# Kernel tuning notes

Hardware: AMD Instinct MI355X
Metric: run time of the kernel (lower is better)

Reference implementation:

```python
import jax, jax.numpy as jnp
import numpy as np

N_SRC0, N_DST0 = 500000, 65536
N_DST1 = 8192
E0, E1 = 1048576, 131072
H = 4
SLOPE = 0.2


def gat_conv(h_src, h_dst, src, dst, Ws, Wd, al, ar, b, n_dst, act):
    # h_src: [Ns, Fin], Ws: [Fin, H*D]
    D = Ws.shape[1] // H
    fs = (h_src @ Ws).reshape(-1, H, D)          # [Ns,H,D]
    fd = (h_dst @ Wd).reshape(-1, H, D)          # [Nd,H,D]
    el = jnp.einsum('nhd,hd->nh', fs, al)        # [Ns,H]
    er = jnp.einsum('nhd,hd->nh', fd, ar)        # [Nd,H]
    e = jax.nn.leaky_relu(el[src] + er[dst], SLOPE)   # [E,H]
    m = jax.ops.segment_max(e, dst, num_segments=n_dst, indices_are_sorted=True)
    a = jnp.exp(e - m[dst])                      # [E,H]
    s = jax.ops.segment_sum(a, dst, num_segments=n_dst, indices_are_sorted=True)
    alpha = a / s[dst]                           # [E,H]
    msg = fs[src] * alpha[..., None]             # [E,H,D]
    out = jax.ops.segment_sum(msg, dst, num_segments=n_dst, indices_are_sorted=True) + b
    return act(out)                              # [Nd,H,D]


def setup_inputs() -> dict:
    key = jax.random.key(0)
    ks = jax.random.split(key, 16)
    D0, D1 = 64, 47
    inp = {
        'x': jax.random.normal(ks[0], (N_SRC0, 128), jnp.float32),
        'src0': jax.random.randint(ks[1], (E0,), 0, N_SRC0, jnp.int32),
        'dst0': jnp.sort(jax.random.randint(ks[2], (E0,), 0, N_DST0, jnp.int32)),
        'src1': jax.random.randint(ks[3], (E1,), 0, N_DST0, jnp.int32),
        'dst1': jnp.sort(jax.random.randint(ks[4], (E1,), 0, N_DST1, jnp.int32)),
        'Ws0': jax.random.normal(ks[5], (128, H * D0), jnp.float32) * 0.05,
        'Wd0': jax.random.normal(ks[6], (128, H * D0), jnp.float32) * 0.05,
        'al0': jax.random.normal(ks[7], (H, D0), jnp.float32) * 0.05,
        'ar0': jax.random.normal(ks[8], (H, D0), jnp.float32) * 0.05,
        'b0': jax.random.normal(ks[9], (H, D0), jnp.float32) * 0.05,
        'Ws1': jax.random.normal(ks[10], (H * D0, H * D1), jnp.float32) * 0.05,
        'Wd1': jax.random.normal(ks[11], (H * D0, H * D1), jnp.float32) * 0.05,
        'al1': jax.random.normal(ks[12], (H, D1), jnp.float32) * 0.05,
        'ar1': jax.random.normal(ks[13], (H, D1), jnp.float32) * 0.05,
        'b1': jax.random.normal(ks[14], (H, D1), jnp.float32) * 0.05,
    }
    return inp


def reference(x, src0, dst0, src1, dst1, Ws0, Wd0, al0, ar0, b0, Ws1, Wd1, al1, ar1, b1):
    # Layer 0: bipartite GATConv with ReLU, flatten heads
    h_dst = x[:N_DST0]
    h = gat_conv(x, h_dst, src0, dst0, Ws0, Wd0, al0, ar0, b0, N_DST0, jax.nn.relu)
    h = h.reshape(N_DST0, -1)                    # [N_DST0, H*D0]
    # Layer 1: no activation, mean over heads, log_softmax
    h_dst = h[:N_DST1]
    h = gat_conv(h, h_dst, src1, dst1, Ws1, Wd1, al1, ar1, b1, N_DST1, lambda z: z)
    h = h.mean(axis=1)                           # [N_DST1, D1]
    return jax.nn.log_softmax(h, axis=-1)
```

## Files before the change

kernel.cpp:

```cpp
#include <hip/hip_runtime.h>

typedef _Float16 half8  __attribute__((ext_vector_type(8)));
typedef _Float16 half4v __attribute__((ext_vector_type(4)));
typedef float    f32x4  __attribute__((ext_vector_type(4)));

#define GAT_SLOPE 0.2f
#define N_SRC0 500000
#define N_DST0 65536
#define N_DST1 8192
#define E0 1048576
#define E1 131072
#define H 4

__device__ __forceinline__ float leaky(float x) { return x >= 0.f ? x : GAT_SLOPE * x; }

__global__ __launch_bounds__(256) void prep_kernel(
    const float* __restrict__ Ws0, const float* __restrict__ Wd0,
    const float* __restrict__ al0, const float* __restrict__ ar0,
    const float* __restrict__ Ws1, const float* __restrict__ Wd1,
    const float* __restrict__ al1, const float* __restrict__ ar1,
    const int* __restrict__ dst0, const int* __restrict__ dst1,
    _Float16* __restrict__ BTs, _Float16* __restrict__ BT0,
    _Float16* __restrict__ WLR0, float* __restrict__ wl1, float* __restrict__ wr1,
    int* __restrict__ seg0, int* __restrict__ seg1) {
  int i = blockIdx.x * 256 + threadIdx.x;
  if (i < 65536) {
    int n = i >> 10, kk = i & 1023, h = kk >> 8, k = kk & 255;
    BTs[i] = (n < 47) ? (_Float16)(0.25f * Ws1[(size_t)k * 188 + h * 47 + n]) : (_Float16)0.f;
    return;
  }
  i -= 65536;
  if (i < 32768) {
    int nrow = i >> 7, k = i & 127;
    BT0[i] = (_Float16)Ws0[(size_t)k * 256 + nrow];
    return;
  }
  i -= 32768;
  if (i < 2048) {
    int n = i >> 7, k = i & 127;
    float v = 0.f;
    if (n < 4) {
      for (int d = 0; d < 64; ++d) v += Ws0[(size_t)k * 256 + n * 64 + d] * al0[n * 64 + d];
    } else if (n < 8) {
      int h = n - 4;
      for (int d = 0; d < 64; ++d) v += Wd0[(size_t)k * 256 + h * 64 + d] * ar0[h * 64 + d];
    }
    WLR0[i] = (_Float16)v;
    return;
  }
  i -= 2048;
  if (i < 1024) {
    int k = i >> 2, h = i & 3;
    float v = 0.f;
    for (int d = 0; d < 47; ++d) v += Ws1[(size_t)k * 188 + h * 47 + d] * al1[h * 47 + d];
    wl1[i] = v;
    return;
  }
  i -= 1024;
  if (i < 1024) {
    int k = i >> 2, h = i & 3;
    float v = 0.f;
    for (int d = 0; d < 47; ++d) v += Wd1[(size_t)k * 188 + h * 47 + d] * ar1[h * 47 + d];
    wr1[i] = v;
    return;
  }
  i -= 1024;
  if (i <= E0) {
    int lo = (i == 0) ? 0 : dst0[i - 1] + 1;
    int hi = (i == E0) ? N_DST0 : dst0[i];
    for (int d = lo; d <= hi; ++d) seg0[d] = i;
    return;
  }
  i -= (E0 + 1);
  if (i <= E1) {
    int lo = (i == 0) ? 0 : dst1[i - 1] + 1;
    int hi = (i == E1) ? N_DST1 : dst1[i];
    for (int d = lo; d <= hi; ++d) seg1[d] = i;
  }
}
#define PREP_TOTAL (65536 + 32768 + 2048 + 1024 + 1024 + (E0 + 1) + (E1 + 1))

__global__ __launch_bounds__(256) void cvt_elr_mfma_kernel(
    const float* __restrict__ x, const _Float16* __restrict__ WLR,
    _Float16* __restrict__ xh, float* __restrict__ el, float* __restrict__ er,
    int M, int n_dst) {
  __shared__ _Float16 As[128 * 128];
  const int t = threadIdx.x, lane = t & 63, wid = t >> 6;
  const int m0 = blockIdx.x * 128;
  for (int i = 0; i < 8; ++i) {
    int c = t + 256 * i;
    int row = c >> 4, j = c & 15;
    int gr = m0 + row;
    half8 va = {};
    if (gr < M) {
      float4 f0 = *(const float4*)(x + (size_t)gr * 128 + j * 8);
      float4 f1 = *(const float4*)(x + (size_t)gr * 128 + j * 8 + 4);
      va[0] = (_Float16)f0.x; va[1] = (_Float16)f0.y;
      va[2] = (_Float16)f0.z; va[3] = (_Float16)f0.w;
      va[4] = (_Float16)f1.x; va[5] = (_Float16)f1.y;
      va[6] = (_Float16)f1.z; va[7] = (_Float16)f1.w;
      *(half8*)(xh + (size_t)gr * 128 + j * 8) = va;
    }
    *(half8*)(&As[row * 128 + ((j ^ (row & 7)) << 3)]) = va;
  }
  half8 bf[4];
  for (int kc = 0; kc < 4; ++kc)
    bf[kc] = *(const half8*)(WLR + (lane & 15) * 128 + kc * 32 + (lane >> 4) * 8);
  __syncthreads();
  f32x4 acc[2] = {};
  for (int rt = 0; rt < 2; ++rt) {
    int row = (wid * 2 + rt) * 16 + (lane & 15);
    for (int kc = 0; kc < 4; ++kc) {
      int chunk = kc * 4 + (lane >> 4);
      half8 af = *(const half8*)(&As[row * 128 + ((chunk ^ (row & 7)) << 3)]);
      acc[rt] = __builtin_amdgcn_mfma_f32_16x16x32_f16(af, bf[kc], acc[rt], 0, 0, 0);
    }
  }
  int col = lane & 15, quad = lane >> 4;
  for (int rt = 0; rt < 2; ++rt)
    for (int r = 0; r < 4; ++r) {
      int row = m0 + (wid * 2 + rt) * 16 + quad * 4 + r;
      if (row < M) {
        if (col < 4) el[(size_t)row * 4 + col] = acc[rt][r];
        else if (col < 8 && row < n_dst) er[(size_t)row * 4 + col - 4] = acc[rt][r];
      }
    }
}

__global__ __launch_bounds__(256) void agg0s_kernel(
    const int* __restrict__ src, const int* __restrict__ seg,
    const float* __restrict__ el, const float* __restrict__ er,
    const _Float16* __restrict__ xh, _Float16* __restrict__ axh) {
  const int lane = threadIdx.x & 63, w = threadIdx.x >> 6;
  const int n = blockIdx.x * 4 + w;
  int s0 = seg[n], len = seg[n + 1] - s0;
  float4 erv = *(const float4*)(er + (size_t)n * 4);
  float a0 = 0.f, a1 = 0.f, a2 = 0.f, a3 = 0.f;
  float t0 = 0.f, t1 = 0.f, t2 = 0.f, t3 = 0.f;
  int sreg = 0;
  if (lane < len) {
    sreg = src[s0 + lane];
    float4 e4 = *(const float4*)(el + (size_t)sreg * 4);
    a0 = __expf(leaky(e4.x + erv.x)); a1 = __expf(leaky(e4.y + erv.y));
    a2 = __expf(leaky(e4.z + erv.z)); a3 = __expf(leaky(e4.w + erv.w));
    t0 = a0; t1 = a1; t2 = a2; t3 = a3;
  }
  for (int idx = 64 + lane; idx < len; idx += 64) {
    int s = src[s0 + idx];
    float4 e4 = *(const float4*)(el + (size_t)s * 4);
    t0 += __expf(leaky(e4.x + erv.x)); t1 += __expf(leaky(e4.y + erv.y));
    t2 += __expf(leaky(e4.z + erv.z)); t3 += __expf(leaky(e4.w + erv.w));
  }
#pragma unroll
  for (int off = 32; off; off >>= 1) {
    t0 += __shfl_xor(t0, off); t1 += __shfl_xor(t1, off);
    t2 += __shfl_xor(t2, off); t3 += __shfl_xor(t3, off);
  }
  float si0 = t0 > 0.f ? 1.f / t0 : 0.f;
  float si1 = t1 > 0.f ? 1.f / t1 : 0.f;
  float si2 = t2 > 0.f ? 1.f / t2 : 0.f;
  float si3 = t3 > 0.f ? 1.f / t3 : 0.f;
  const int g = lane >> 5, ci = lane & 31;
  float A[4][4] = {};
  int iters = (len + 1) >> 1;
  for (int k = 0; k < iters; ++k) {
    int idx = g + 2 * k;
    int sl = idx < 64 ? idx : 0;
    float ah0 = __shfl(a0, sl), ah1 = __shfl(a1, sl);
    float ah2 = __shfl(a2, sl), ah3 = __shfl(a3, sl);
    int sidx = __shfl(sreg, sl);
    if (idx >= 64 && idx < len) {
      sidx = src[s0 + idx];
      float4 e4 = *(const float4*)(el + (size_t)sidx * 4);
      ah0 = __expf(leaky(e4.x + erv.x)); ah1 = __expf(leaky(e4.y + erv.y));
      ah2 = __expf(leaky(e4.z + erv.z)); ah3 = __expf(leaky(e4.w + erv.w));
    }
    if (idx < len) {
      half4v xv = *(const half4v*)(xh + (size_t)sidx * 128 + ci * 4);
#pragma unroll
      for (int c = 0; c < 4; ++c) {
        float xc = (float)xv[c];
        A[0][c] += ah0 * xc; A[1][c] += ah1 * xc;
        A[2][c] += ah2 * xc; A[3][c] += ah3 * xc;
      }
    }
  }
#pragma unroll
  for (int h = 0; h < 4; ++h)
#pragma unroll
    for (int c = 0; c < 4; ++c) A[h][c] += __shfl_xor(A[h][c], 32);
  if (g == 0) {
    float si[4] = {si0, si1, si2, si3};
#pragma unroll
    for (int h = 0; h < 4; ++h) {
      half4v o;
#pragma unroll
      for (int c = 0; c < 4; ++c) o[c] = (_Float16)(A[h][c] * si[h]);
      *(half4v*)(axh + ((size_t)n * 4 + h) * 128 + ci * 4) = o;
    }
  }
}

__global__ __launch_bounds__(256) void agg1s_kernel(
    const int* __restrict__ src, const int* __restrict__ seg,
    const float* __restrict__ el, const float* __restrict__ er,
    const _Float16* __restrict__ h0, _Float16* __restrict__ axh1) {
  const int lane = threadIdx.x & 63, w = threadIdx.x >> 6;
  const int n = blockIdx.x * 4 + w;
  int s0 = seg[n], len = seg[n + 1] - s0;
  float4 erv = *(const float4*)(er + (size_t)n * 4);
  float a0 = 0.f, a1 = 0.f, a2 = 0.f, a3 = 0.f;
  float t0 = 0.f, t1 = 0.f, t2 = 0.f, t3 = 0.f;
  int sreg = 0;
  if (lane < len) {
    sreg = src[s0 + lane];
    float4 e4 = *(const float4*)(el + (size_t)sreg * 4);
    a0 = __expf(leaky(e4.x + erv.x)); a1 = __expf(leaky(e4.y + erv.y));
    a2 = __expf(leaky(e4.z + erv.z)); a3 = __expf(leaky(e4.w + erv.w));
    t0 = a0; t1 = a1; t2 = a2; t3 = a3;
  }
  for (int idx = 64 + lane; idx < len; idx += 64) {
    int s = src[s0 + idx];
    float4 e4 = *(const float4*)(el + (size_t)s * 4);
    t0 += __expf(leaky(e4.x + erv.x)); t1 += __expf(leaky(e4.y + erv.y));
    t2 += __expf(leaky(e4.z + erv.z)); t3 += __expf(leaky(e4.w + erv.w));
  }
#pragma unroll
  for (int off = 32; off; off >>= 1) {
    t0 += __shfl_xor(t0, off); t1 += __shfl_xor(t1, off);
    t2 += __shfl_xor(t2, off); t3 += __shfl_xor(t3, off);
  }
  float si0 = t0 > 0.f ? 1.f / t0 : 0.f;
  float si1 = t1 > 0.f ? 1.f / t1 : 0.f;
  float si2 = t2 > 0.f ? 1.f / t2 : 0.f;
  float si3 = t3 > 0.f ? 1.f / t3 : 0.f;
  const int g = lane >> 5, ci = lane & 31;
  float A[4][8] = {};
  int iters = (len + 1) >> 1;
  for (int k = 0; k < iters; ++k) {
    int idx = g + 2 * k;
    int sl = idx < 64 ? idx : 0;
    float ah0 = __shfl(a0, sl), ah1 = __shfl(a1, sl);
    float ah2 = __shfl(a2, sl), ah3 = __shfl(a3, sl);
    int sidx = __shfl(sreg, sl);
    if (idx >= 64 && idx < len) {
      sidx = src[s0 + idx];
      float4 e4 = *(const float4*)(el + (size_t)sidx * 4);
      ah0 = __expf(leaky(e4.x + erv.x)); ah1 = __expf(leaky(e4.y + erv.y));
      ah2 = __expf(leaky(e4.z + erv.z)); ah3 = __expf(leaky(e4.w + erv.w));
    }
    if (idx < len) {
      half8 xv = *(const half8*)(h0 + (size_t)sidx * 256 + ci * 8);
#pragma unroll
      for (int c = 0; c < 8; ++c) {
        float xc = (float)xv[c];
        A[0][c] += ah0 * xc; A[1][c] += ah1 * xc;
        A[2][c] += ah2 * xc; A[3][c] += ah3 * xc;
      }
    }
  }
#pragma unroll
  for (int h = 0; h < 4; ++h)
#pragma unroll
    for (int c = 0; c < 8; ++c) A[h][c] += __shfl_xor(A[h][c], 32);
  if (g == 0) {
    float si[4] = {si0, si1, si2, si3};
#pragma unroll
    for (int h = 0; h < 4; ++h) {
      half8 o;
#pragma unroll
      for (int c = 0; c < 8; ++c) o[c] = (_Float16)(A[h][c] * si[h]);
      *(half8*)(axh1 + ((size_t)n * 4 + h) * 256 + ci * 8) = o;
    }
  }
}

__global__ __launch_bounds__(256) void gemm_h0_kernel(
    const _Float16* __restrict__ axh, const _Float16* __restrict__ BT,
    const float* __restrict__ b, const float* __restrict__ wl1,
    const float* __restrict__ wr1, _Float16* __restrict__ h0,
    float* __restrict__ el1, float* __restrict__ er1) {
  __shared__ _Float16 As[128 * 128];
  __shared__ _Float16 Bs[64 * 128];
  const int t = threadIdx.x, lane = t & 63, wid = t >> 6;
  const int m0 = blockIdx.x * 128;
  const int cl = lane & 15, quad = lane >> 4;
  const int wm = wid * 32;
  f32x4 el1p[2][4] = {}, er1p[2][4] = {};
  for (int h = 0; h < 4; ++h) {
    for (int i = 0; i < 8; ++i) {
      int c = t + 256 * i, row = c >> 4, j = c & 15;
      int sw = ((j ^ (row & 7)) << 3);
      *(half8*)(&As[row * 128 + sw]) =
          *(const half8*)(axh + ((size_t)(m0 + row) * 4 + h) * 128 + j * 8);
    }
    for (int i = 0; i < 4; ++i) {
      int c = t + 256 * i, row = c >> 4, j = c & 15;
      int sw = ((j ^ (row & 7)) << 3);
      *(half8*)(&Bs[row * 128 + sw]) =
          *(const half8*)(BT + (size_t)(h * 64 + row) * 128 + j * 8);
    }
    __syncthreads();
    f32x4 acc[2][4] = {};
    for (int ks = 0; ks < 4; ++ks) {
      int kc = ks * 4 + quad;
      half8 af[2], bf[4];
      for (int i = 0; i < 2; ++i) {
        int ra = wm + 16 * i + cl;
        af[i] = *(const half8*)(&As[ra * 128 + ((kc ^ (ra & 7)) << 3)]);
      }
      for (int j2 = 0; j2 < 4; ++j2) {
        int rb = 16 * j2 + cl;
        bf[j2] = *(const half8*)(&Bs[rb * 128 + ((kc ^ (rb & 7)) << 3)]);
      }
      for (int i = 0; i < 2; ++i)
        for (int j2 = 0; j2 < 4; ++j2)
          acc[i][j2] = __builtin_amdgcn_mfma_f32_16x16x32_f16(af[i], bf[j2], acc[i][j2], 0, 0, 0);
    }
    __syncthreads();
    for (int j2 = 0; j2 < 4; ++j2) {
      int gcol = h * 64 + 16 * j2 + cl;
      float bias = b[gcol];
      f32x4 wlv = *(const f32x4*)(wl1 + (size_t)gcol * 4);
      f32x4 wrv = *(const f32x4*)(wr1 + (size_t)gcol * 4);
      for (int i = 0; i < 2; ++i) {
        int r0 = m0 + wm + 16 * i + quad * 4;
        for (int r = 0; r < 4; ++r) {
          float v = fmaxf(acc[i][j2][r] + bias, 0.f);
          h0[(size_t)(r0 + r) * 256 + gcol] = (_Float16)v;
          el1p[i][r] += wlv * v;
          er1p[i][r] += wrv * v;
        }
      }
    }
  }
#pragma unroll
  for (int off = 1; off < 16; off <<= 1)
#pragma unroll
    for (int i = 0; i < 2; ++i)
#pragma unroll
      for (int r = 0; r < 4; ++r)
#pragma unroll
        for (int c = 0; c < 4; ++c) {
          el1p[i][r][c] += __shfl_xor(el1p[i][r][c], off);
          er1p[i][r][c] += __shfl_xor(er1p[i][r][c], off);
        }
  if (cl == 0) {
    for (int i = 0; i < 2; ++i)
      for (int r = 0; r < 4; ++r) {
        int row = m0 + wm + 16 * i + quad * 4 + r;
        *(f32x4*)(el1 + (size_t)row * 4) = el1p[i][r];
        if (row < N_DST1) *(f32x4*)(er1 + (size_t)row * 4) = er1p[i][r];
      }
  }
}

__global__ __launch_bounds__(256) void gemm_out_kernel(
    const _Float16* __restrict__ axh1, const _Float16* __restrict__ BTs,
    const float* __restrict__ b1, float* __restrict__ out) {
  __shared__ _Float16 As[64 * 128];
  __shared__ _Float16 Bs[64 * 128];
  const int t = threadIdx.x, lane = t & 63, wid = t >> 6;
  const int m0 = blockIdx.x * 64;
  f32x4 acc[4] = {};
  for (int k0 = 0; k0 < 1024; k0 += 128) {
    for (int i = 0; i < 4; ++i) {
      int c = t + 256 * i, row = c >> 4, j = c & 15;
      int sw = ((j ^ (row & 7)) << 3);
      *(half8*)(&As[row * 128 + sw]) =
          *(const half8*)(axh1 + (size_t)(m0 + row) * 1024 + k0 + j * 8);
      *(half8*)(&Bs[row * 128 + sw]) =
          *(const half8*)(BTs + (size_t)row * 1024 + k0 + j * 8);
    }
    __syncthreads();
    const int wm = wid * 16;
    for (int ks = 0; ks < 4; ++ks) {
      int kc = ks * 4 + (lane >> 4);
      int ra = wm + (lane & 15);
      half8 af = *(const half8*)(&As[ra * 128 + ((kc ^ (ra & 7)) << 3)]);
      for (int j2 = 0; j2 < 4; ++j2) {
        int rb = 16 * j2 + (lane & 15);
        half8 bf = *(const half8*)(&Bs[rb * 128 + ((kc ^ (rb & 7)) << 3)]);
        acc[j2] = __builtin_amdgcn_mfma_f32_16x16x32_f16(af, bf, acc[j2], 0, 0, 0);
      }
    }
    __syncthreads();
  }
  int quad = lane >> 4, cl = lane & 15;
  float bm[3];
  for (int j2 = 0; j2 < 3; ++j2) {
    int col = 16 * j2 + cl;
    bm[j2] = (col < 47) ? 0.25f * (b1[col] + b1[col + 47] + b1[col + 94] + b1[col + 141]) : 0.f;
  }
  for (int r = 0; r < 4; ++r) {
    int row = m0 + wid * 16 + quad * 4 + r;
    float v[3];
    float mx = -1e30f;
    for (int j2 = 0; j2 < 3; ++j2) {
      int col = 16 * j2 + cl;
      v[j2] = acc[j2][r] + bm[j2];
      if (col < 47) mx = fmaxf(mx, v[j2]);
    }
    for (int off = 8; off; off >>= 1) mx = fmaxf(mx, __shfl_xor(mx, off));
    float s = 0.f;
    for (int j2 = 0; j2 < 3; ++j2) {
      int col = 16 * j2 + cl;
      if (col < 47) s += __expf(v[j2] - mx);
    }
    for (int off = 8; off; off >>= 1) s += __shfl_xor(s, off);
    float lse = mx + __logf(s);
    for (int j2 = 0; j2 < 3; ++j2) {
      int col = 16 * j2 + cl;
      if (col < 47) out[(size_t)row * 47 + col] = v[j2] - lse;
    }
  }
}

extern "C" void kernel_launch(void* const* d_in, const int* in_sizes, int n_in,
                              void* d_out, int out_size, void* d_ws, size_t ws_size,
                              hipStream_t stream) {
  const float* x   = (const float*)d_in[0];
  const int* src0  = (const int*)d_in[1];
  const int* dst0  = (const int*)d_in[2];
  const int* src1  = (const int*)d_in[3];
  const int* dst1  = (const int*)d_in[4];
  const float* Ws0 = (const float*)d_in[5];
  const float* Wd0 = (const float*)d_in[6];
  const float* al0 = (const float*)d_in[7];
  const float* ar0 = (const float*)d_in[8];
  const float* b0  = (const float*)d_in[9];
  const float* Ws1 = (const float*)d_in[10];
  const float* Wd1 = (const float*)d_in[11];
  const float* al1 = (const float*)d_in[12];
  const float* ar1 = (const float*)d_in[13];
  const float* b1  = (const float*)d_in[14];

  char* w = (char*)d_ws;
  auto alloc = [&](size_t bytes) {
    char* p = w;
    w += (bytes + 255) & ~(size_t)255;
    return p;
  };
  _Float16* xh   = (_Float16*)alloc((size_t)N_SRC0 * 128 * 2);
  _Float16* axh  = (_Float16*)alloc((size_t)N_DST0 * 512 * 2);
  _Float16* h0   = (_Float16*)alloc((size_t)N_DST0 * 256 * 2);
  _Float16* axh1 = (_Float16*)alloc((size_t)N_DST1 * 1024 * 2);
  float* el0     = (float*)alloc((size_t)N_SRC0 * 4 * 4);
  float* er0     = (float*)alloc((size_t)N_DST0 * 4 * 4);
  float* el1     = (float*)alloc((size_t)N_DST0 * 4 * 4);
  float* er1     = (float*)alloc((size_t)N_DST1 * 4 * 4);
  int* seg0      = (int*)alloc((size_t)(N_DST0 + 1) * 4);
  int* seg1      = (int*)alloc((size_t)(N_DST1 + 1) * 4);
  _Float16* BT0  = (_Float16*)alloc(256 * 128 * 2);
  _Float16* BTs  = (_Float16*)alloc(64 * 1024 * 2);
  _Float16* WLR0 = (_Float16*)alloc(16 * 128 * 2);
  float* wl1     = (float*)alloc(256 * 4 * 4);
  float* wr1     = (float*)alloc(256 * 4 * 4);

  prep_kernel<<<(PREP_TOTAL + 255) / 256, 256, 0, stream>>>(
      Ws0, Wd0, al0, ar0, Ws1, Wd1, al1, ar1, dst0, dst1,
      BTs, BT0, WLR0, wl1, wr1, seg0, seg1);
  cvt_elr_mfma_kernel<<<(N_SRC0 + 127) / 128, 256, 0, stream>>>(x, WLR0, xh, el0, er0,
                                                                N_SRC0, N_DST0);
  agg0s_kernel<<<N_DST0 / 4, 256, 0, stream>>>(src0, seg0, el0, er0, xh, axh);
  gemm_h0_kernel<<<N_DST0 / 128, 256, 0, stream>>>(axh, BT0, b0, wl1, wr1, h0, el1, er1);
  agg1s_kernel<<<N_DST1 / 4, 256, 0, stream>>>(src1, seg1, el1, er1, h0, axh1);
  gemm_out_kernel<<<N_DST1 / 64, 256, 0, stream>>>(axh1, BTs, b1, (float*)d_out);
}
```

Measured before the change: 544.3 us.

## Fuse layer-0 attention aggregation with the per-head projection GEMM

Merges the layer-0 edge aggregation kernel and the h0 GEMM into a single 512-thread kernel. Each block aggregates 64 destination nodes into shared memory, using 16 lanes per node with half8 loads, then runs the MFMA projection directly from LDS with one head per wave pair. This removes the 64 MB fp16 axh intermediate write and read plus one kernel launch. In exchange it reads B fragments straight from global memory, reduces el1/er1 through LDS atomics, and cuts per-node edge parallelism from 64 lanes to 16, which lengthens the serial per-edge loop.

New measurement: 600.6 us. 10.3% more time.

```diff
diff --git a/kernel.cpp b/kernel.cpp
--- a/kernel.cpp
+++ b/kernel.cpp
@@ -127,77 +127,163 @@
     }
 }
 
-__global__ __launch_bounds__(256) void agg0s_kernel(
+__global__ __launch_bounds__(512) void agg_gemm0_kernel(
     const int* __restrict__ src, const int* __restrict__ seg,
     const float* __restrict__ el, const float* __restrict__ er,
-    const _Float16* __restrict__ xh, _Float16* __restrict__ axh) {
-  const int lane = threadIdx.x & 63, w = threadIdx.x >> 6;
-  const int n = blockIdx.x * 4 + w;
-  int s0 = seg[n], len = seg[n + 1] - s0;
-  float4 erv = *(const float4*)(er + (size_t)n * 4);
-  float a0 = 0.f, a1 = 0.f, a2 = 0.f, a3 = 0.f;
-  float t0 = 0.f, t1 = 0.f, t2 = 0.f, t3 = 0.f;
-  int sreg = 0;
-  if (lane < len) {
-    sreg = src[s0 + lane];
-    float4 e4 = *(const float4*)(el + (size_t)sreg * 4);
-    a0 = __expf(leaky(e4.x + erv.x)); a1 = __expf(leaky(e4.y + erv.y));
-    a2 = __expf(leaky(e4.z + erv.z)); a3 = __expf(leaky(e4.w + erv.w));
-    t0 = a0; t1 = a1; t2 = a2; t3 = a3;
-  }
-  for (int idx = 64 + lane; idx < len; idx += 64) {
-    int s = src[s0 + idx];
-    float4 e4 = *(const float4*)(el + (size_t)s * 4);
-    t0 += __expf(leaky(e4.x + erv.x)); t1 += __expf(leaky(e4.y + erv.y));
-    t2 += __expf(leaky(e4.z + erv.z)); t3 += __expf(leaky(e4.w + erv.w));
-  }
-#pragma unroll
-  for (int off = 32; off; off >>= 1) {
-    t0 += __shfl_xor(t0, off); t1 += __shfl_xor(t1, off);
-    t2 += __shfl_xor(t2, off); t3 += __shfl_xor(t3, off);
-  }
-  float si0 = t0 > 0.f ? 1.f / t0 : 0.f;
-  float si1 = t1 > 0.f ? 1.f / t1 : 0.f;
-  float si2 = t2 > 0.f ? 1.f / t2 : 0.f;
-  float si3 = t3 > 0.f ? 1.f / t3 : 0.f;
-  const int g = lane >> 5, ci = lane & 31;
-  float A[4][4] = {};
-  int iters = (len + 1) >> 1;
-  for (int k = 0; k < iters; ++k) {
-    int idx = g + 2 * k;
-    int sl = idx < 64 ? idx : 0;
-    float ah0 = __shfl(a0, sl), ah1 = __shfl(a1, sl);
-    float ah2 = __shfl(a2, sl), ah3 = __shfl(a3, sl);
-    int sidx = __shfl(sreg, sl);
-    if (idx >= 64 && idx < len) {
-      sidx = src[s0 + idx];
-      float4 e4 = *(const float4*)(el + (size_t)sidx * 4);
-      ah0 = __expf(leaky(e4.x + erv.x)); ah1 = __expf(leaky(e4.y + erv.y));
-      ah2 = __expf(leaky(e4.z + erv.z)); ah3 = __expf(leaky(e4.w + erv.w));
-    }
-    if (idx < len) {
-      half4v xv = *(const half4v*)(xh + (size_t)sidx * 128 + ci * 4);
-#pragma unroll
-      for (int c = 0; c < 4; ++c) {
+    const _Float16* __restrict__ xh, const _Float16* __restrict__ BT,
+    const float* __restrict__ b, const float* __restrict__ wl1,
+    const float* __restrict__ wr1, _Float16* __restrict__ h0,
+    float* __restrict__ el1, float* __restrict__ er1) {
+  __shared__ _Float16 As[4 * 64 * 128];
+  __shared__ float elds[64][8];
+  const int t = threadIdx.x, lane = t & 63, wid = t >> 6;
+  const int m0 = blockIdx.x * 64;
+  const int g = lane >> 4, ci = lane & 15;
+  if (t < 128) ((float4*)elds)[t] = float4{0.f, 0.f, 0.f, 0.f};
+
+  for (int rnd = 0; rnd < 2; ++rnd) {
+    const int j = rnd * 32 + wid * 4 + g;
+    const int n = m0 + j;
+    int s0 = seg[n], len = seg[n + 1] - s0;
+    float4 erv = *(const float4*)(er + (size_t)n * 4);
+    float a0[4], a1[4], a2[4], a3[4];
+    int sr[4];
+    float t0 = 0.f, t1 = 0.f, t2 = 0.f, t3 = 0.f;
+#pragma unroll
+    for (int jj = 0; jj < 4; ++jj) {
+      int idx = ci + jj * 16;
+      float v0 = 0.f, v1 = 0.f, v2 = 0.f, v3 = 0.f;
+      int sv = 0;
+      if (idx < len) {
+        sv = src[s0 + idx];
+        float4 e4 = *(const float4*)(el + (size_t)sv * 4);
+        v0 = __expf(leaky(e4.x + erv.x)); v1 = __expf(leaky(e4.y + erv.y));
+        v2 = __expf(leaky(e4.z + erv.z)); v3 = __expf(leaky(e4.w + erv.w));
+        t0 += v0; t1 += v1; t2 += v2; t3 += v3;
+      }
+      a0[jj] = v0; a1[jj] = v1; a2[jj] = v2; a3[jj] = v3; sr[jj] = sv;
+    }
+    for (int idx = ci + 64; idx < len; idx += 16) {
+      int sv = src[s0 + idx];
+      float4 e4 = *(const float4*)(el + (size_t)sv * 4);
+      t0 += __expf(leaky(e4.x + erv.x)); t1 += __expf(leaky(e4.y + erv.y));
+      t2 += __expf(leaky(e4.z + erv.z)); t3 += __expf(leaky(e4.w + erv.w));
+    }
+#pragma unroll
+    for (int off = 8; off; off >>= 1) {
+      t0 += __shfl_xor(t0, off); t1 += __shfl_xor(t1, off);
+      t2 += __shfl_xor(t2, off); t3 += __shfl_xor(t3, off);
+    }
+    float si0 = t0 > 0.f ? 1.f / t0 : 0.f;
+    float si1 = t1 > 0.f ? 1.f / t1 : 0.f;
+    float si2 = t2 > 0.f ? 1.f / t2 : 0.f;
+    float si3 = t3 > 0.f ? 1.f / t3 : 0.f;
+    float A[4][8] = {};
+    for (int k = 0; k < len; ++k) {
+      float ah0, ah1, ah2, ah3;
+      int sidx;
+      if (k < 64) {
+        int jj = k >> 4, sl = (g << 4) | (k & 15);
+        if (jj == 0) {
+          ah0 = __shfl(a0[0], sl); ah1 = __shfl(a1[0], sl);
+          ah2 = __shfl(a2[0], sl); ah3 = __shfl(a3[0], sl); sidx = __shfl(sr[0], sl);
+        } else if (jj == 1) {
+          ah0 = __shfl(a0[1], sl); ah1 = __shfl(a1[1], sl);
+          ah2 = __shfl(a2[1], sl); ah3 = __shfl(a3[1], sl); sidx = __shfl(sr[1], sl);
+        } else if (jj == 2) {
+          ah0 = __shfl(a0[2], sl); ah1 = __shfl(a1[2], sl);
+          ah2 = __shfl(a2[2], sl); ah3 = __shfl(a3[2], sl); sidx = __shfl(sr[2], sl);
+        } else {
+          ah0 = __shfl(a0[3], sl); ah1 = __shfl(a1[3], sl);
+          ah2 = __shfl(a2[3], sl); ah3 = __shfl(a3[3], sl); sidx = __shfl(sr[3], sl);
+        }
+      } else {
+        sidx = src[s0 + k];
+        float4 e4 = *(const float4*)(el + (size_t)sidx * 4);
+        ah0 = __expf(leaky(e4.x + erv.x)); ah1 = __expf(leaky(e4.y + erv.y));
+        ah2 = __expf(leaky(e4.z + erv.z)); ah3 = __expf(leaky(e4.w + erv.w));
+      }
+      half8 xv = *(const half8*)(xh + (size_t)sidx * 128 + ci * 8);
+#pragma unroll
+      for (int c = 0; c < 8; ++c) {
         float xc = (float)xv[c];
         A[0][c] += ah0 * xc; A[1][c] += ah1 * xc;
         A[2][c] += ah2 * xc; A[3][c] += ah3 * xc;
       }
     }
-  }
-#pragma unroll
-  for (int h = 0; h < 4; ++h)
-#pragma unroll
-    for (int c = 0; c < 4; ++c) A[h][c] += __shfl_xor(A[h][c], 32);
-  if (g == 0) {
     float si[4] = {si0, si1, si2, si3};
 #pragma unroll
     for (int h = 0; h < 4; ++h) {
-      half4v o;
-#pragma unroll
-      for (int c = 0; c < 4; ++c) o[c] = (_Float16)(A[h][c] * si[h]);
-      *(half4v*)(axh + ((size_t)n * 4 + h) * 128 + ci * 4) = o;
-    }
+      half8 o;
+#pragma unroll
+      for (int c = 0; c < 8; ++c) o[c] = (_Float16)(A[h][c] * si[h]);
+      *(half8*)(&As[(h * 64 + j) * 128 + ((ci ^ (j & 7)) << 3)]) = o;
+    }
+  }
+  __syncthreads();
+
+  const int h = wid >> 1, wi = wid & 1;
+  const int cl = ci, quad = g;
+  const bool need_er = (m0 < N_DST1);
+  f32x4 acc[2][4] = {};
+  for (int ks = 0; ks < 4; ++ks) {
+    int kc = ks * 4 + quad;
+    half8 af[2], bf[4];
+    for (int i = 0; i < 2; ++i) {
+      int ra = wi * 32 + 16 * i + cl;
+      af[i] = *(const half8*)(&As[(h * 64 + ra) * 128 + ((kc ^ (ra & 7)) << 3)]);
+    }
+    for (int j2 = 0; j2 < 4; ++j2) {
+      int rb = 16 * j2 + cl;
+      bf[j2] = *(const half8*)(BT + (size_t)(h * 64 + rb) * 128 + kc * 8);
+    }
+    for (int i = 0; i < 2; ++i)
+      for (int j2 = 0; j2 < 4; ++j2)
+        acc[i][j2] = __builtin_amdgcn_mfma_f32_16x16x32_f16(af[i], bf[j2], acc[i][j2], 0, 0, 0);
+  }
+  f32x4 el1p[2][4] = {}, er1p[2][4] = {};
+  for (int j2 = 0; j2 < 4; ++j2) {
+    int gcol = h * 64 + 16 * j2 + cl;
+    float bias = b[gcol];
+    f32x4 wlv = *(const f32x4*)(wl1 + (size_t)gcol * 4);
+    f32x4 wrv = *(const f32x4*)(wr1 + (size_t)gcol * 4);
+    for (int i = 0; i < 2; ++i) {
+      int r0 = m0 + wi * 32 + 16 * i + quad * 4;
+      for (int r = 0; r < 4; ++r) {
+        float v = fmaxf(acc[i][j2][r] + bias, 0.f);
+        h0[(size_t)(r0 + r) * 256 + gcol] = (_Float16)v;
+        el1p[i][r] += wlv * v;
+        if (need_er) er1p[i][r] += wrv * v;
+      }
+    }
+  }
+#pragma unroll
+  for (int off = 1; off < 16; off <<= 1)
+#pragma unroll
+    for (int i = 0; i < 2; ++i)
+#pragma unroll
+      for (int r = 0; r < 4; ++r)
+#pragma unroll
+        for (int c = 0; c < 4; ++c) {
+          el1p[i][r][c] += __shfl_xor(el1p[i][r][c], off);
+          if (need_er) er1p[i][r][c] += __shfl_xor(er1p[i][r][c], off);
+        }
+  if (cl == 0) {
+    for (int i = 0; i < 2; ++i)
+      for (int r = 0; r < 4; ++r) {
+        int rl = wi * 32 + 16 * i + quad * 4 + r;
+#pragma unroll
+        for (int hh = 0; hh < 4; ++hh) {
+          atomicAdd(&elds[rl][hh], el1p[i][r][hh]);
+          if (need_er) atomicAdd(&elds[rl][4 + hh], er1p[i][r][hh]);
+        }
+      }
+  }
+  __syncthreads();
+  if (t < 128) {
+    int r = t >> 1, half = t & 1, row = m0 + r;
+    if (half == 0) *(float4*)(el1 + (size_t)row * 4) = *(float4*)&elds[r][0];
+    else if (row < N_DST1) *(float4*)(er1 + (size_t)row * 4) = *(float4*)&elds[r][4];
   }
 }
 
@@ -275,86 +361,6 @@
   }
 }
 
-__global__ __launch_bounds__(256) void gemm_h0_kernel(
-    const _Float16* __restrict__ axh, const _Float16* __restrict__ BT,
-    const float* __restrict__ b, const float* __restrict__ wl1,
-    const float* __restrict__ wr1, _Float16* __restrict__ h0,
-    float* __restrict__ el1, float* __restrict__ er1) {
-  __shared__ _Float16 As[128 * 128];
-  __shared__ _Float16 Bs[64 * 128];
-  const int t = threadIdx.x, lane = t & 63, wid = t >> 6;
-  const int m0 = blockIdx.x * 128;
-  const int cl = lane & 15, quad = lane >> 4;
-  const int wm = wid * 32;
-  f32x4 el1p[2][4] = {}, er1p[2][4] = {};
-  for (int h = 0; h < 4; ++h) {
-    for (int i = 0; i < 8; ++i) {
-      int c = t + 256 * i, row = c >> 4, j = c & 15;
-      int sw = ((j ^ (row & 7)) << 3);
-      *(half8*)(&As[row * 128 + sw]) =
-          *(const half8*)(axh + ((size_t)(m0 + row) * 4 + h) * 128 + j * 8);
-    }
-    for (int i = 0; i < 4; ++i) {
-      int c = t + 256 * i, row = c >> 4, j = c & 15;
-      int sw = ((j ^ (row & 7)) << 3);
-      *(half8*)(&Bs[row * 128 + sw]) =
-          *(const half8*)(BT + (size_t)(h * 64 + row) * 128 + j * 8);
-    }
-    __syncthreads();
-    f32x4 acc[2][4] = {};
-    for (int ks = 0; ks < 4; ++ks) {
-      int kc = ks * 4 + quad;
-      half8 af[2], bf[4];
-      for (int i = 0; i < 2; ++i) {
-        int ra = wm + 16 * i + cl;
-        af[i] = *(const half8*)(&As[ra * 128 + ((kc ^ (ra & 7)) << 3)]);
-      }
-      for (int j2 = 0; j2 < 4; ++j2) {
-        int rb = 16 * j2 + cl;
-        bf[j2] = *(const half8*)(&Bs[rb * 128 + ((kc ^ (rb & 7)) << 3)]);
-      }
-      for (int i = 0; i < 2; ++i)
-        for (int j2 = 0; j2 < 4; ++j2)
-          acc[i][j2] = __builtin_amdgcn_mfma_f32_16x16x32_f16(af[i], bf[j2], acc[i][j2], 0, 0, 0);
-    }
-    __syncthreads();
-    for (int j2 = 0; j2 < 4; ++j2) {
-      int gcol = h * 64 + 16 * j2 + cl;
-      float bias = b[gcol];
-      f32x4 wlv = *(const f32x4*)(wl1 + (size_t)gcol * 4);
-      f32x4 wrv = *(const f32x4*)(wr1 + (size_t)gcol * 4);
-      for (int i = 0; i < 2; ++i) {
-        int r0 = m0 + wm + 16 * i + quad * 4;
-        for (int r = 0; r < 4; ++r) {
-          float v = fmaxf(acc[i][j2][r] + bias, 0.f);
-          h0[(size_t)(r0 + r) * 256 + gcol] = (_Float16)v;
-          el1p[i][r] += wlv * v;
-          er1p[i][r] += wrv * v;
-        }
-      }
-    }
-  }
-#pragma unroll
-  for (int off = 1; off < 16; off <<= 1)
-#pragma unroll
-    for (int i = 0; i < 2; ++i)
-#pragma unroll
-      for (int r = 0; r < 4; ++r)
-#pragma unroll
-        for (int c = 0; c < 4; ++c) {
-          el1p[i][r][c] += __shfl_xor(el1p[i][r][c], off);
-          er1p[i][r][c] += __shfl_xor(er1p[i][r][c], off);
-        }
-  if (cl == 0) {
-    for (int i = 0; i < 2; ++i)
-      for (int r = 0; r < 4; ++r) {
-        int row = m0 + wm + 16 * i + quad * 4 + r;
-        *(f32x4*)(el1 + (size_t)row * 4) = el1p[i][r];
-        if (row < N_DST1) *(f32x4*)(er1 + (size_t)row * 4) = er1p[i][r];
-      }
-  }
-}
-
 __global__ __launch_bounds__(256) void gemm_out_kernel(
     const _Float16* __restrict__ axh1, const _Float16* __restrict__ BTs,
     const float* __restrict__ b1, float* __restrict__ out) {
@@ -442,7 +448,6 @@
     return p;
   };
   _Float16* xh   = (_Float16*)alloc((size_t)N_SRC0 * 128 * 2);
-  _Float16* axh  = (_Float16*)alloc((size_t)N_DST0 * 512 * 2);
   _Float16* h0   = (_Float16*)alloc((size_t)N_DST0 * 256 * 2);
   _Float16* axh1 = (_Float16*)alloc((size_t)N_DST1 * 1024 * 2);
   float* el0     = (float*)alloc((size_t)N_SRC0 * 4 * 4);
@@ -462,8 +467,8 @@
       BTs, BT0, WLR0, wl1, wr1, seg0, seg1);
   cvt_elr_mfma_kernel<<<(N_SRC0 + 127) / 128, 256, 0, stream>>>(x, WLR0, xh, el0, er0,
                                                                 N_SRC0, N_DST0);
-  agg0s_kernel<<<N_DST0 / 4, 256, 0, stream>>>(src0, seg0, el0, er0, xh, axh);
-  gemm_h0_kernel<<<N_DST0 / 128, 256, 0, stream>>>(axh, BT0, b0, wl1, wr1, h0, el1, er1);
+  agg_gemm0_kernel<<<N_DST0 / 64, 512, 0, stream>>>(src0, seg0, el0, er0, xh, BT0, b0,
+                                                    wl1, wr1, h0, el1, er1);
   agg1s_kernel<<<N_DST1 / 4, 256, 0, stream>>>(src1, seg1, el1, er1, h0, axh1);
   gemm_out_kernel<<<N_DST1 / 64, 256, 0, stream>>>(axh1, BTs, b1, (float*)d_out);
 }
```
